# Optimization experiments

Measured on AMD Instinct MI355X. Metric: run time of the kernel, lower is better.

The kernel has to match this reference:

```python
import jax, jax.numpy as jnp
import numpy as np

EPS_BN = 1e-5

def conv1(W, x):
    # 1x1 conv1d, no bias: W (Cout,Cin), x (B,Cin,N)
    return jnp.einsum('oc,bcn->bon', W, x)

def bn(x, g, b):
    # training-mode BatchNorm1d over (batch, points) per channel
    m = jnp.mean(x, axis=(0, 2), keepdims=True)
    v = jnp.mean((x - m) ** 2, axis=(0, 2), keepdims=True)
    return g[None, :, None] * (x - m) / jnp.sqrt(v + EPS_BN) + b[None, :, None]

def three_interpolation(p_dense, p_sparse, f_sparse):
    # p_dense (B,N1,3), p_sparse (B,N2,3), f_sparse (B,C,N2) -> (B,C,N1)
    d2 = jnp.sum((p_dense[:, :, None, :] - p_sparse[:, None, :, :]) ** 2, axis=-1)  # (B,N1,N2)
    neg, idx = jax.lax.top_k(-d2, 3)  # 3 nearest neighbors, (B,N1,3)
    w = 1.0 / (jnp.maximum(-neg, 0.0) + 1e-8)  # inverse (squared) distance, as pointnet2 three_nn
    w = w / jnp.sum(w, axis=-1, keepdims=True)
    gathered = jax.vmap(lambda f, i: f[:, i])(f_sparse, idx)  # (B,C,N1,3)
    return jnp.einsum('bcnk,bnk->bcn', gathered, w)

def fp(p_dense, f_skip, p_sparse, f_sparse, W1, g1, b1, W2, g2, b2):
    # FeaturePropogation upsample branch: concat(skip, interp) -> [conv1d+BN] x decoder_layers (act_args=None)
    x = jnp.concatenate([f_skip, three_interpolation(p_dense, p_sparse, f_sparse)], axis=1)
    x = bn(conv1(W1, x), g1, b1)
    x = bn(conv1(W2, x), g2, b2)
    return x

def setup_inputs():
    key = jax.random.key(0)
    ks = iter(jax.random.split(key, 40))
    B, N = 4, 8192
    Ns = [N, N, 2048, 512, 128]      # point counts of p0..p4 (strides 4)
    Cs = [128, 256, 512, 1024]       # encoder_channel_list
    d = {}
    for i in range(5):
        d[f'p{i}'] = jax.random.normal(next(ks), (B, Ns[i], 3), jnp.float32)
    for i in range(4):
        d[f'f{i + 1}'] = jax.random.normal(next(ks), (B, Cs[i], Ns[i + 1]), jnp.float32)
    d['cls_label'] = jax.random.randint(next(ks), (B, 1), 0, 16)
    # class-label convs: 16 -> 64 (BN+GELU) -> C0
    d['Wc1'] = jax.random.normal(next(ks), (64, 16), jnp.float32) * 0.1
    d['gc'] = jax.random.uniform(next(ks), (64,), jnp.float32, 0.5, 1.5)
    d['bc'] = jax.random.normal(next(ks), (64,), jnp.float32) * 0.1
    d['Wc2'] = jax.random.normal(next(ks), (Cs[0], 64), jnp.float32) * 0.1
    # decoder stages, coarsest (s2) to finest (s0)
    ins = [Cs[2] + Cs[3], Cs[1] + Cs[2], Cs[0] + Cs[1]]
    outs = [Cs[2], Cs[1], Cs[0]]
    for tag, ci, co in zip(['s2', 's1', 's0'], ins, outs):
        d[f'W{tag}a'] = jax.random.normal(next(ks), (co, ci), jnp.float32) * 0.05
        d[f'g{tag}a'] = jax.random.uniform(next(ks), (co,), jnp.float32, 0.5, 1.5)
        d[f'b{tag}a'] = jax.random.normal(next(ks), (co,), jnp.float32) * 0.1
        d[f'W{tag}b'] = jax.random.normal(next(ks), (co, co), jnp.float32) * 0.05
        d[f'g{tag}b'] = jax.random.uniform(next(ks), (co,), jnp.float32, 0.5, 1.5)
        d[f'b{tag}b'] = jax.random.normal(next(ks), (co,), jnp.float32) * 0.1
    return d

def reference(p0, p1, p2, p3, p4, f1, f2, f3, f4, cls_label,
              Wc1, gc, bc, Wc2,
              Ws2a, gs2a, bs2a, Ws2b, gs2b, bs2b,
              Ws1a, gs1a, bs1a, Ws1b, gs1b, bs1b,
              Ws0a, gs0a, bs0a, Ws0b, gs0b, bs0b):
    B, N = p0.shape[0], p0.shape[1]
    # one-hot class embedding broadcast over points, mapped 16 -> 64 -> C0
    one_hot = jax.nn.one_hot(cls_label[:, 0], 16, dtype=f1.dtype)  # (B,16)
    cls_feat = jnp.broadcast_to(one_hot[:, :, None], (B, 16, N))
    cls_feat = conv1(Wc2, jax.nn.gelu(bn(conv1(Wc1, cls_feat), gc, bc), approximate=False))
    # decoder stages, coarse to fine
    f3n = fp(p3, f3, p4, f4, Ws2a, gs2a, bs2a, Ws2b, gs2b, bs2b)   # (B,512,512)
    f2n = fp(p2, f2, p3, f3n, Ws1a, gs1a, bs1a, Ws1b, gs1b, bs1b)  # (B,256,2048)
    f1n = fp(p1, f1 + cls_feat, p2, f2n, Ws0a, gs0a, bs0a, Ws0b, gs0b, bs0b)  # (B,128,8192)
    return f1n
```

## Files before the change

kernel.cpp:

```cpp
#include <hip/hip_runtime.h>
#include <math.h>

#define BN_EPS 1e-5f

typedef float f32x4 __attribute__((ext_vector_type(4)));
typedef short s16x8 __attribute__((ext_vector_type(8)));
typedef short s16x4 __attribute__((ext_vector_type(4)));

__device__ __forceinline__ unsigned short f2bf(float f) {
    unsigned u = __builtin_bit_cast(unsigned, f);
    u = u + 0x7FFFu + ((u >> 16) & 1u);
    return (unsigned short)(u >> 16);
}
__device__ __forceinline__ float bf2f(unsigned short s) {
    unsigned u = ((unsigned)s) << 16;
    return __builtin_bit_cast(float, u);
}

__device__ __forceinline__ void gload16(const void* g, void* l) {
    __builtin_amdgcn_global_load_lds((const __attribute__((address_space(1))) unsigned int*)g,
                                     (__attribute__((address_space(3))) unsigned int*)l,
                                     16, 0, 0);
}

__global__ __launch_bounds__(256) void tr_all(const float* __restrict__ f1,
                                              const float* __restrict__ f2,
                                              const float* __restrict__ f3,
                                              const float* __restrict__ f4,
                                              unsigned short* __restrict__ F1T,
                                              unsigned short* __restrict__ F2T,
                                              unsigned short* __restrict__ F3T,
                                              unsigned short* __restrict__ F4T,
                                              const int* __restrict__ lbl,
                                              const float* __restrict__ Wc1,
                                              const float* __restrict__ gc,
                                              const float* __restrict__ bc,
                                              const float* __restrict__ Wc2) {
    __shared__ float t[32][33];
    __shared__ float clsv[32];
    __shared__ float hsh[4][64];
    __shared__ float actsh[4][64];
    int bx = blockIdx.x, b = blockIdx.y;
    const float* in; unsigned short* out; int C, N, nx, seg; bool docls = false;
    if (bx < 128)      { in = f4; out = F4T; C = 1024; N = 128;  nx = 4;   seg = bx; }
    else if (bx < 384) { in = f3; out = F3T; C = 512;  N = 512;  nx = 16;  seg = bx - 128; }
    else if (bx < 896) { in = f2; out = F2T; C = 256;  N = 2048; nx = 64;  seg = bx - 384; }
    else               { in = f1; out = F1T; C = 128;  N = 8192; nx = 256; seg = bx - 896; docls = true; }
    int n0 = (seg % nx) * 32, c0 = (seg / nx) * 32;
    int tid = threadIdx.x;
    if (docls) {
        { int b2 = tid >> 6, c = tid & 63; hsh[b2][c] = Wc1[c * 16 + lbl[b2]]; }
        __syncthreads();
        if (tid < 64) {
            int c = tid;
            float m = 0.f;
            for (int b2 = 0; b2 < 4; b2++) m += hsh[b2][c];
            m *= 0.25f;
            float v = 0.f;
            for (int b2 = 0; b2 < 4; b2++) { float d = hsh[b2][c] - m; v += d * d; }
            v *= 0.25f;
            float sc = gc[c] * rsqrtf(v + BN_EPS);
            float sh = bc[c] - m * sc;
            for (int b2 = 0; b2 < 4; b2++) {
                float x = hsh[b2][c] * sc + sh;
                actsh[b2][c] = 0.5f * x * (1.f + erff(x * 0.70710678118654752f));
            }
        }
        __syncthreads();
        if (tid < 32) {
            float s = 0.f;
            for (int c = 0; c < 64; c++) s += Wc2[(size_t)(c0 + tid) * 64 + c] * actsh[b][c];
            clsv[tid] = s;
        }
        __syncthreads();
    }
    int i = tid & 31, jj = tid >> 5;
#pragma unroll
    for (int j = jj; j < 32; j += 8) {
        float v = in[((size_t)b * C + c0 + j) * N + n0 + i];
        if (docls) v += clsv[j];
        t[j][i] = v;
    }
    __syncthreads();
    int j2 = tid & 31, i2b = tid >> 5;
#pragma unroll
    for (int i2 = i2b; i2 < 32; i2 += 8)
        out[((size_t)b * N + n0 + i2) * C + c0 + j2] = f2bf(t[j2][i2]);
}

template<int CAND, int CHUNK, int STRIDE, bool PART>
__device__ __forceinline__ void knn_body(const float* __restrict__ pd,
                                         const float* __restrict__ ps,
                                         int N1, int N2total, int grp, int slice, int b,
                                         int* __restrict__ idx, float* __restrict__ w,
                                         unsigned long long* __restrict__ pk, int nslice,
                                         float* spx, float* spy, float* spz) {
    int tid = threadIdx.x;
    int cbase = slice * CAND;
    for (int g = tid; g < CAND; g += 256) {
        int s = g / CHUNK, off = g % CHUNK;
        size_t base = ((size_t)b * N2total + cbase + g) * 3;
        spx[s * STRIDE + off] = ps[base];
        spy[s * STRIDE + off] = ps[base + 1];
        spz[s * STRIDE + off] = ps[base + 2];
    }
    __syncthreads();
    int sub = tid & 7;
    int n = grp * 32 + (tid >> 3);
    size_t pb = ((size_t)b * N1 + n) * 3;
    float px = pd[pb], py = pd[pb + 1], pz = pd[pb + 2];
    float dd0 = 3.4e38f, dd1 = 3.4e38f, dd2 = 3.4e38f;
    int ii0 = 0, ii1 = 0, ii2 = 0;
    const float* rx = spx + sub * STRIDE;
    const float* ry = spy + sub * STRIDE;
    const float* rz = spz + sub * STRIDE;
    int jbase = cbase + sub * CHUNK;
    for (int t = 0; t < CHUNK; t += 4) {
        f32x4 x4 = *(const f32x4*)(rx + t);
        f32x4 y4 = *(const f32x4*)(ry + t);
        f32x4 z4 = *(const f32x4*)(rz + t);
#pragma unroll
        for (int e = 0; e < 4; e++) {
            float dx = px - x4[e], dy = py - y4[e], dz = pz - z4[e];
            float d = dx * dx + dy * dy + dz * dz;
            int j = jbase + t + e;
            bool C0 = d < dd0, C1 = d < dd1, C2 = d < dd2;
            int ni2 = C1 ? ii1 : (C2 ? j : ii2);
            int ni1 = C0 ? ii0 : (C1 ? j : ii1);
            int ni0 = C0 ? j : ii0;
            dd2 = __builtin_amdgcn_fmed3f(d, dd1, dd2);
            dd1 = __builtin_amdgcn_fmed3f(d, dd0, dd1);
            dd0 = fminf(d, dd0);
            ii0 = ni0; ii1 = ni1; ii2 = ni2;
        }
    }
    unsigned long long k0 = ((unsigned long long)__builtin_bit_cast(unsigned, dd0) << 32) | (unsigned)ii0;
    unsigned long long k1 = ((unsigned long long)__builtin_bit_cast(unsigned, dd1) << 32) | (unsigned)ii1;
    unsigned long long k2 = ((unsigned long long)__builtin_bit_cast(unsigned, dd2) << 32) | (unsigned)ii2;
#pragma unroll
    for (int m = 1; m < 8; m <<= 1) {
        unsigned long long e0, e1, e2;
        { int lo = __shfl_xor((int)(unsigned)(k0 & 0xFFFFFFFFull), m), hi = __shfl_xor((int)(unsigned)(k0 >> 32), m);
          e0 = ((unsigned long long)(unsigned)hi << 32) | (unsigned)lo; }
        { int lo = __shfl_xor((int)(unsigned)(k1 & 0xFFFFFFFFull), m), hi = __shfl_xor((int)(unsigned)(k1 >> 32), m);
          e1 = ((unsigned long long)(unsigned)hi << 32) | (unsigned)lo; }
        { int lo = __shfl_xor((int)(unsigned)(k2 & 0xFFFFFFFFull), m), hi = __shfl_xor((int)(unsigned)(k2 >> 32), m);
          e2 = ((unsigned long long)(unsigned)hi << 32) | (unsigned)lo; }
        unsigned long long t0, t1;
        t0 = k0 > e0 ? k0 : e0; k0 = k0 < e0 ? k0 : e0; t1 = k1 > t0 ? k1 : t0; k1 = k1 < t0 ? k1 : t0; k2 = k2 < t1 ? k2 : t1;
        t0 = k0 > e1 ? k0 : e1; k0 = k0 < e1 ? k0 : e1; t1 = k1 > t0 ? k1 : t0; k1 = k1 < t0 ? k1 : t0; k2 = k2 < t1 ? k2 : t1;
        t0 = k0 > e2 ? k0 : e2; k0 = k0 < e2 ? k0 : e2; t1 = k1 > t0 ? k1 : t0; k1 = k1 < t0 ? k1 : t0; k2 = k2 < t1 ? k2 : t1;
    }
    if (sub == 0) {
        if (PART) {
            size_t o = ((size_t)(b * N1 + n) * nslice + slice) * 3;
            pk[o] = k0; pk[o + 1] = k1; pk[o + 2] = k2;
        } else {
            float f0 = __builtin_bit_cast(float, (unsigned)(k0 >> 32));
            float f1 = __builtin_bit_cast(float, (unsigned)(k1 >> 32));
            float f2 = __builtin_bit_cast(float, (unsigned)(k2 >> 32));
            float w0 = 1.f / (f0 + 1e-8f), w1 = 1.f / (f1 + 1e-8f), w2 = 1.f / (f2 + 1e-8f);
            float s = 1.f / (w0 + w1 + w2);
            size_t o = ((size_t)b * N1 + n) * 3;
            idx[o] = (int)(unsigned)(k0 & 0xFFFFFFFFull);
            idx[o + 1] = (int)(unsigned)(k1 & 0xFFFFFFFFull);
            idx[o + 2] = (int)(unsigned)(k2 & 0xFFFFFFFFull);
            w[o] = w0 * s; w[o + 1] = w1 * s; w[o + 2] = w2 * s;
        }
    }
}

__global__ __launch_bounds__(256) void knn_part(const float* __restrict__ p1,
                                                const float* __restrict__ p2,
                                                const float* __restrict__ p3,
                                                const float* __restrict__ p4,
                                                int* __restrict__ idx1, float* __restrict__ w1,
                                                int* __restrict__ idx2, float* __restrict__ w2,
                                                unsigned long long* __restrict__ pk0) {
    __shared__ float spx[8 * 72], spy[8 * 72], spz[8 * 72];
    int bx = blockIdx.x, b = blockIdx.y;
    if (bx < 16)      knn_body<128, 16, 24, false>(p3, p4, 512, 128, bx, 0, b, idx2, w2, nullptr, 1, spx, spy, spz);
    else if (bx < 80) knn_body<512, 64, 72, false>(p2, p3, 2048, 512, bx - 16, 0, b, idx1, w1, nullptr, 1, spx, spy, spz);
    else {
        int u = bx - 80;
        knn_body<512, 64, 72, true>(p1, p2, 8192, 2048, u >> 2, u & 3, b, nullptr, nullptr, pk0, 4, spx, spy, spz);
    }
}

__global__ __launch_bounds__(256) void knn_merge(const unsigned long long* __restrict__ pk,
                                                 int* __restrict__ idx, float* __restrict__ w,
                                                 int NQ) {
    int q = blockIdx.x * 256 + threadIdx.x;
    if (q >= NQ) return;
    const unsigned long long* p = pk + (size_t)q * 12;
    unsigned long long k0 = ~0ull, k1 = ~0ull, k2 = ~0ull;
#pragma unroll
    for (int i = 0; i < 12; i++) {
        unsigned long long c = p[i];
        unsigned long long t0 = k0 > c ? k0 : c; k0 = k0 < c ? k0 : c;
        unsigned long long t1 = k1 > t0 ? k1 : t0; k1 = k1 < t0 ? k1 : t0;
        k2 = k2 < t1 ? k2 : t1;
    }
    float f0 = __builtin_bit_cast(float, (unsigned)(k0 >> 32));
    float f1 = __builtin_bit_cast(float, (unsigned)(k1 >> 32));
    float f2 = __builtin_bit_cast(float, (unsigned)(k2 >> 32));
    float w0 = 1.f / (f0 + 1e-8f), w1 = 1.f / (f1 + 1e-8f), w2 = 1.f / (f2 + 1e-8f);
    float s = 1.f / (w0 + w1 + w2);
    size_t o = (size_t)q * 3;
    idx[o] = (int)(unsigned)(k0 & 0xFFFFFFFFull);
    idx[o + 1] = (int)(unsigned)(k1 & 0xFFFFFFFFull);
    idx[o + 2] = (int)(unsigned)(k2 & 0xFFFFFFFFull);
    w[o] = w0 * s; w[o + 1] = w1 * s; w[o + 2] = w2 * s;
}

__global__ __launch_bounds__(256) void interp_y(const unsigned short* __restrict__ GT,
                                                const int* __restrict__ idx,
                                                const float* __restrict__ w,
                                                unsigned short* __restrict__ out,
                                                int M, int N1, int N2) {
    int mq = M >> 3;
    size_t gid = (size_t)blockIdx.x * 256 + threadIdx.x;
    if (gid >= (size_t)4 * N1 * mq) return;
    int c = (int)(gid % mq) * 8;
    int n = (int)((gid / mq) % N1);
    int b = (int)(gid / ((size_t)mq * N1));
    size_t ob = ((size_t)b * N1 + n) * 3;
    int i0 = idx[ob], i1 = idx[ob + 1], i2 = idx[ob + 2];
    float w0 = w[ob], w1 = w[ob + 1], w2 = w[ob + 2];
    s16x8 v0 = *(const s16x8*)(GT + ((size_t)b * N2 + i0) * M + c);
    s16x8 v1 = *(const s16x8*)(GT + ((size_t)b * N2 + i1) * M + c);
    s16x8 v2 = *(const s16x8*)(GT + ((size_t)b * N2 + i2) * M + c);
    s16x8 o;
#pragma unroll
    for (int j = 0; j < 8; j++) {
        float v = w0 * bf2f((unsigned short)v0[j]) + w1 * bf2f((unsigned short)v1[j]) + w2 * bf2f((unsigned short)v2[j]);
        o[j] = (short)f2bf(v);
    }
    *(s16x8*)(out + ((size_t)b * N1 + n) * M + c) = o;
}

__global__ __launch_bounds__(256) void wprep(const float* __restrict__ W,
                                             const float* __restrict__ sc,
                                             const float* __restrict__ sh,
                                             unsigned short* __restrict__ Wb,
                                             float* __restrict__ bias,
                                             int Ktot, int kOff, int Ks) {
    int m = blockIdx.x;
    int tid = threadIdx.x;
    float bsum = 0.f;
    for (int k = tid; k < Ks; k += 256) {
        float wv = W[(size_t)m * Ktot + kOff + k];
        float o = wv;
        if (sc) {
            o = wv * sc[k];
            bsum += wv * sh[k];
        }
        Wb[(size_t)m * Ks + k] = f2bf(o);
    }
    __shared__ float ls[256];
    ls[tid] = bsum;
    __syncthreads();
    for (int o = 128; o > 0; o >>= 1) {
        if (tid < o) ls[tid] += ls[tid + o];
        __syncthreads();
    }
    if (tid == 0) bias[m] = ls[0];
}

template<bool PRE>
__global__ __launch_bounds__(256) void gemm64(const unsigned short* __restrict__ XT,
                                              const unsigned short* __restrict__ Wb,
                                              const float* __restrict__ bias,
                                              const unsigned short* __restrict__ pre,
                                              unsigned short* __restrict__ OutT,
                                              float* __restrict__ ps,
                                              int BN, int K, int M) {
    __shared__ unsigned short As[2][64 * 32];
    __shared__ unsigned short Bs[2][64 * 32];
    __shared__ float sred[2][2][32][2];
    int tid = threadIdx.x;
    int lane = tid & 63, wid = tid >> 6;
    int wn = wid & 1, wm = wid >> 1;
    int bx = blockIdx.x, by = blockIdx.y;

    int srow = (wid << 4) + (lane >> 2);
    int skcol = (lane & 3) << 3;
    const unsigned short* gA = XT + (size_t)(bx * 64 + srow) * K + skcol;
    const unsigned short* gB = Wb + (size_t)(by * 64 + srow) * K + skcol;

    int r16 = lane & 15, q = lane >> 4;
    f32x4 acc[2][2];
    if (PRE) {
        const unsigned short* Pb = pre + (size_t)(bx * 64) * M + by * 64;
#pragma unroll
        for (int i = 0; i < 2; i++)
#pragma unroll
            for (int j = 0; j < 2; j++) {
                int mcol = wm * 32 + j * 16 + r16;
#pragma unroll
                for (int r = 0; r < 4; r++) {
                    int n = wn * 32 + i * 16 + q * 4 + r;
                    acc[i][j][r] = bf2f(Pb[(size_t)n * M + mcol]);
                }
            }
    } else {
#pragma unroll
        for (int i = 0; i < 2; i++)
#pragma unroll
            for (int j = 0; j < 2; j++) acc[i][j] = (f32x4)0.f;
    }

    int nt = K >> 5;
    gload16(gA, &As[0][wid * 512]);
    gload16(gB, &Bs[0][wid * 512]);

    for (int t = 0; t < nt; t++) {
        int cur = t & 1;
        if (t + 1 < nt) {
            int k0 = (t + 1) << 5;
            gload16(gA + k0, &As[cur ^ 1][wid * 512]);
            gload16(gB + k0, &Bs[cur ^ 1][wid * 512]);
            asm volatile("s_waitcnt vmcnt(2)" ::: "memory");
        } else {
            asm volatile("s_waitcnt vmcnt(0)" ::: "memory");
        }
        __syncthreads();
        s16x8 afr[2], bfr[2];
        afr[0] = *(const s16x8*)&As[cur][(wn * 32 + r16) * 32 + q * 8];
        afr[1] = *(const s16x8*)&As[cur][(wn * 32 + 16 + r16) * 32 + q * 8];
        bfr[0] = *(const s16x8*)&Bs[cur][(wm * 32 + r16) * 32 + q * 8];
        bfr[1] = *(const s16x8*)&Bs[cur][(wm * 32 + 16 + r16) * 32 + q * 8];
        asm volatile("s_waitcnt lgkmcnt(0)" ::: "memory");
        __builtin_amdgcn_sched_barrier(0);
        __syncthreads();
#pragma unroll
        for (int i = 0; i < 2; i++)
#pragma unroll
            for (int j = 0; j < 2; j++)
                acc[i][j] = __builtin_amdgcn_mfma_f32_16x16x32_bf16(afr[i], bfr[j], acc[i][j], 0, 0, 0);
    }

    int mc0 = by * 64 + wm * 32 + r16;
    float bv[2] = { bias[mc0], bias[mc0 + 16] };
    unsigned short* Ob = OutT + (size_t)(bx * 64) * M + by * 64;
    float s[2] = {0.f, 0.f}, qq[2] = {0.f, 0.f};
#pragma unroll
    for (int i = 0; i < 2; i++) {
#pragma unroll
        for (int j = 0; j < 2; j++) {
            int mcol = wm * 32 + j * 16 + r16;
#pragma unroll
            for (int r = 0; r < 4; r++) {
                float v = acc[i][j][r] + bv[j];
                s[j] += v; qq[j] += v * v;
                int n = wn * 32 + i * 16 + q * 4 + r;
                Ob[(size_t)n * M + mcol] = f2bf(v);
            }
        }
    }
#pragma unroll
    for (int j = 0; j < 2; j++) {
        s[j] += __shfl_xor(s[j], 16); s[j] += __shfl_xor(s[j], 32);
        qq[j] += __shfl_xor(qq[j], 16); qq[j] += __shfl_xor(qq[j], 32);
    }
    if (lane < 16) {
#pragma unroll
        for (int j = 0; j < 2; j++) {
            sred[wn][wm][j * 16 + lane][0] = s[j];
            sred[wn][wm][j * 16 + lane][1] = qq[j];
        }
    }
    __syncthreads();
    if (tid < 64) {
        int wmm = tid >> 5, c = tid & 31;
        float ssum = sred[0][wmm][c][0] + sred[1][wmm][c][0];
        float qsum = sred[0][wmm][c][1] + sred[1][wmm][c][1];
        size_t blin = (size_t)by * gridDim.x + bx;
        ps[blin * 128 + tid * 2] = ssum;
        ps[blin * 128 + tid * 2 + 1] = qsum;
    }
}

__global__ __launch_bounds__(256) void bn_finalize(const float* __restrict__ ps,
                                                   const float* __restrict__ g,
                                                   const float* __restrict__ bb,
                                                   float* __restrict__ sc,
                                                   float* __restrict__ sh,
                                                   int gx, int Npts) {
    int m = blockIdx.x;
    int by = m >> 6, ch = m & 63;
    float s = 0.f, q = 0.f;
    for (int bxi = threadIdx.x; bxi < gx; bxi += 256) {
        size_t blin = (size_t)by * gx + bxi;
        s += ps[blin * 128 + ch * 2];
        q += ps[blin * 128 + ch * 2 + 1];
    }
    __shared__ float ls[256], lq[256];
    ls[threadIdx.x] = s; lq[threadIdx.x] = q;
    __syncthreads();
    for (int o = 128; o > 0; o >>= 1) {
        if (threadIdx.x < o) { ls[threadIdx.x] += ls[threadIdx.x + o]; lq[threadIdx.x] += lq[threadIdx.x + o]; }
        __syncthreads();
    }
    if (threadIdx.x == 0) {
        float inv = 1.f / (float)Npts;
        float mean = ls[0] * inv;
        float var = fmaxf(lq[0] * inv - mean * mean, 0.f);
        float scale = g[m] * rsqrtf(var + BN_EPS);
        sc[m] = scale;
        sh[m] = bb[m] - mean * scale;
    }
}

__global__ __launch_bounds__(256) void out_bn_tr(const unsigned short* __restrict__ in,
                                                 float* __restrict__ out,
                                                 const float* __restrict__ sc,
                                                 const float* __restrict__ sh,
                                                 int M, int N) {
    __shared__ float t[32][33];
    int b = blockIdx.z;
    int n0 = blockIdx.x * 32, m0 = blockIdx.y * 32;
    int j = threadIdx.x & 31, ii = threadIdx.x >> 5;
#pragma unroll
    for (int i = ii; i < 32; i += 8)
        t[i][j] = bf2f(in[((size_t)b * N + n0 + i) * M + m0 + j]);
    __syncthreads();
    int i2 = threadIdx.x & 31, j2b = threadIdx.x >> 5;
#pragma unroll
    for (int j2 = j2b; j2 < 32; j2 += 8)
        out[((size_t)b * M + m0 + j2) * N + n0 + i2] = t[i2][j2] * sc[m0 + j2] + sh[m0 + j2];
}

extern "C" void kernel_launch(void* const* d_in, const int* in_sizes, int n_in,
                              void* d_out, int out_size, void* d_ws, size_t ws_size,
                              hipStream_t stream) {
    const float* p1 = (const float*)d_in[1];
    const float* p2 = (const float*)d_in[2];
    const float* p3 = (const float*)d_in[3];
    const float* p4 = (const float*)d_in[4];
    const float* f1 = (const float*)d_in[5];
    const float* f2 = (const float*)d_in[6];
    const float* f3 = (const float*)d_in[7];
    const float* f4 = (const float*)d_in[8];
    const int* cls = (const int*)d_in[9];
    const float* Wc1 = (const float*)d_in[10];
    const float* gc  = (const float*)d_in[11];
    const float* bc  = (const float*)d_in[12];
    const float* Wc2 = (const float*)d_in[13];
    const float* Ws2a = (const float*)d_in[14];
    const float* gs2a = (const float*)d_in[15];
    const float* bs2a = (const float*)d_in[16];
    const float* Ws2b = (const float*)d_in[17];
    const float* gs2b = (const float*)d_in[18];
    const float* bs2b = (const float*)d_in[19];
    const float* Ws1a = (const float*)d_in[20];
    const float* gs1a = (const float*)d_in[21];
    const float* bs1a = (const float*)d_in[22];
    const float* Ws1b = (const float*)d_in[23];
    const float* gs1b = (const float*)d_in[24];
    const float* bs1b = (const float*)d_in[25];
    const float* Ws0a = (const float*)d_in[26];
    const float* gs0a = (const float*)d_in[27];
    const float* bs0a = (const float*)d_in[28];
    const float* Ws0b = (const float*)d_in[29];
    const float* gs0b = (const float*)d_in[30];
    const float* bs0b = (const float*)d_in[31];

    char* ws = (char*)d_ws;
    size_t off = 0;
    auto alloc = [&](size_t bytes) { char* p = ws + off; off += (bytes + 255) & ~(size_t)255; return p; };
    unsigned short* F4T = (unsigned short*)alloc((size_t)4 * 128 * 1024 * 2);
    unsigned short* F3T = (unsigned short*)alloc((size_t)4 * 512 * 512 * 2);
    unsigned short* F2T = (unsigned short*)alloc((size_t)4 * 2048 * 256 * 2);
    unsigned short* F1T = (unsigned short*)alloc((size_t)4 * 8192 * 128 * 2);
    unsigned short* G2T = (unsigned short*)alloc((size_t)4 * 128 * 512 * 2);
    unsigned short* G1T = (unsigned short*)alloc((size_t)4 * 512 * 256 * 2);
    unsigned short* G0T = (unsigned short*)alloc((size_t)4 * 2048 * 128 * 2);
    unsigned short* YI2 = (unsigned short*)alloc((size_t)4 * 512 * 512 * 2);
    unsigned short* YI1 = (unsigned short*)alloc((size_t)4 * 2048 * 256 * 2);
    unsigned short* YI0 = (unsigned short*)alloc((size_t)4 * 8192 * 128 * 2);
    unsigned short* YA  = (unsigned short*)alloc((size_t)4 * 8192 * 128 * 2);
    unsigned short* FN2 = (unsigned short*)alloc((size_t)4 * 512 * 512 * 2);
    unsigned short* FN1 = (unsigned short*)alloc((size_t)4 * 2048 * 256 * 2);
    unsigned short* XO  = (unsigned short*)alloc((size_t)4 * 8192 * 128 * 2);
    unsigned short* WI2 = (unsigned short*)alloc((size_t)512 * 1024 * 2);
    unsigned short* WS2 = (unsigned short*)alloc((size_t)512 * 512 * 2);
    unsigned short* WB2b = (unsigned short*)alloc((size_t)512 * 512 * 2);
    unsigned short* WI1 = (unsigned short*)alloc((size_t)256 * 512 * 2);
    unsigned short* WS1 = (unsigned short*)alloc((size_t)256 * 256 * 2);
    unsigned short* WB1b = (unsigned short*)alloc((size_t)256 * 256 * 2);
    unsigned short* WI0 = (unsigned short*)alloc((size_t)128 * 256 * 2);
    unsigned short* WS0 = (unsigned short*)alloc((size_t)128 * 128 * 2);
    unsigned short* WB0b = (unsigned short*)alloc((size_t)128 * 128 * 2);
    float* BIA2 = (float*)alloc(512 * 4); float* BIS2 = (float*)alloc(512 * 4);
    float* BI2b = (float*)alloc(512 * 4);
    float* BIA1 = (float*)alloc(256 * 4); float* BIS1 = (float*)alloc(256 * 4);
    float* BI1b = (float*)alloc(256 * 4);
    float* BIA0 = (float*)alloc(128 * 4); float* BIS0 = (float*)alloc(128 * 4);
    float* BI0b = (float*)alloc(128 * 4);
    int*   IDX0 = (int*)alloc((size_t)4 * 8192 * 3 * 4);
    float* WGT0 = (float*)alloc((size_t)4 * 8192 * 3 * 4);
    int*   IDX1 = (int*)alloc((size_t)4 * 2048 * 3 * 4);
    float* WGT1 = (float*)alloc((size_t)4 * 2048 * 3 * 4);
    int*   IDX2 = (int*)alloc((size_t)4 * 512 * 3 * 4);
    float* WGT2 = (float*)alloc((size_t)4 * 512 * 3 * 4);
    unsigned long long* PK0 = (unsigned long long*)alloc((size_t)4 * 8192 * 4 * 3 * 8);
    float* PS = (float*)alloc((size_t)1024 * 128 * 4);
    float* SC2a = (float*)alloc(512 * 4); float* SH2a = (float*)alloc(512 * 4);
    float* SC2b = (float*)alloc(512 * 4); float* SH2b = (float*)alloc(512 * 4);
    float* SC1a = (float*)alloc(512 * 4); float* SH1a = (float*)alloc(512 * 4);
    float* SC1b = (float*)alloc(512 * 4); float* SH1b = (float*)alloc(512 * 4);
    float* SC0a = (float*)alloc(512 * 4); float* SH0a = (float*)alloc(512 * 4);
    float* SC0b = (float*)alloc(512 * 4); float* SH0b = (float*)alloc(512 * 4);
    float* OUT = (float*)d_out;

    tr_all<<<dim3(1920, 4), 256, 0, stream>>>(f1, f2, f3, f4, F1T, F2T, F3T, F4T, cls, Wc1, gc, bc, Wc2);
    knn_part<<<dim3(1104, 4), 256, 0, stream>>>(p1, p2, p3, p4, IDX1, WGT1, IDX2, WGT2, PK0);
    knn_merge<<<(4 * 8192) / 256, 256, 0, stream>>>(PK0, IDX0, WGT0, 4 * 8192);
    wprep<<<512, 256, 0, stream>>>(Ws2a, nullptr, nullptr, WI2, BIA2, 1536, 512, 1024);
    wprep<<<512, 256, 0, stream>>>(Ws2a, nullptr, nullptr, WS2, BIS2, 1536, 0, 512);
    wprep<<<256, 256, 0, stream>>>(Ws1a, nullptr, nullptr, WS1, BIS1, 768, 0, 256);
    wprep<<<128, 256, 0, stream>>>(Ws0a, nullptr, nullptr, WS0, BIS0, 384, 0, 128);

    gemm64<false><<<dim3(8, 8), 256, 0, stream>>>(F4T, WI2, BIA2, nullptr, G2T, PS, 512, 1024, 512);
    interp_y<<<(4 * 512 * (512 / 8) + 255) / 256, 256, 0, stream>>>(G2T, IDX2, WGT2, YI2, 512, 512, 128);
    gemm64<true><<<dim3(32, 8), 256, 0, stream>>>(F3T, WS2, BIS2, YI2, YA, PS, 2048, 512, 512);
    bn_finalize<<<512, 256, 0, stream>>>(PS, gs2a, bs2a, SC2a, SH2a, 32, 2048);
    wprep<<<512, 256, 0, stream>>>(Ws2b, SC2a, SH2a, WB2b, BI2b, 512, 0, 512);
    gemm64<false><<<dim3(32, 8), 256, 0, stream>>>(YA, WB2b, BI2b, nullptr, FN2, PS, 2048, 512, 512);
    bn_finalize<<<512, 256, 0, stream>>>(PS, gs2b, bs2b, SC2b, SH2b, 32, 2048);

    wprep<<<256, 256, 0, stream>>>(Ws1a, SC2b, SH2b, WI1, BIA1, 768, 256, 512);
    gemm64<false><<<dim3(32, 4), 256, 0, stream>>>(FN2, WI1, BIA1, nullptr, G1T, PS, 2048, 512, 256);
    interp_y<<<(4 * 2048 * (256 / 8) + 255) / 256, 256, 0, stream>>>(G1T, IDX1, WGT1, YI1, 256, 2048, 512);
    gemm64<true><<<dim3(128, 4), 256, 0, stream>>>(F2T, WS1, BIS1, YI1, YA, PS, 8192, 256, 256);
    bn_finalize<<<256, 256, 0, stream>>>(PS, gs1a, bs1a, SC1a, SH1a, 128, 8192);
    wprep<<<256, 256, 0, stream>>>(Ws1b, SC1a, SH1a, WB1b, BI1b, 256, 0, 256);
    gemm64<false><<<dim3(128, 4), 256, 0, stream>>>(YA, WB1b, BI1b, nullptr, FN1, PS, 8192, 256, 256);
    bn_finalize<<<256, 256, 0, stream>>>(PS, gs1b, bs1b, SC1b, SH1b, 128, 8192);

    wprep<<<128, 256, 0, stream>>>(Ws0a, SC1b, SH1b, WI0, BIA0, 384, 128, 256);
    gemm64<false><<<dim3(128, 2), 256, 0, stream>>>(FN1, WI0, BIA0, nullptr, G0T, PS, 8192, 256, 128);
    interp_y<<<(4 * 8192 * (128 / 8) + 255) / 256, 256, 0, stream>>>(G0T, IDX0, WGT0, YI0, 128, 8192, 2048);
    gemm64<true><<<dim3(512, 2), 256, 0, stream>>>(F1T, WS0, BIS0, YI0, YA, PS, 32768, 128, 128);
    bn_finalize<<<128, 256, 0, stream>>>(PS, gs0a, bs0a, SC0a, SH0a, 512, 32768);
    wprep<<<128, 256, 0, stream>>>(Ws0b, SC0a, SH0a, WB0b, BI0b, 128, 0, 128);
    gemm64<false><<<dim3(512, 2), 256, 0, stream>>>(YA, WB0b, BI0b, nullptr, XO, PS, 32768, 128, 128);
    bn_finalize<<<128, 256, 0, stream>>>(PS, gs0b, bs0b, SC0b, SH0b, 512, 32768);

    out_bn_tr<<<dim3(8192 / 32, 128 / 32, 4), 256, 0, stream>>>(XO, OUT, SC0b, SH0b, 128, 8192);
}
```

Measured before the change: 205.6 us.

## Fuse prep kernels, gather interpolation into GEMM epilogue, last-block BN finalize

Transpose, kNN and the first-layer weight conversion now run in one prep launch. The three-NN interpolation gather moves into the GEMM epilogue, so the separate interp_y kernel and its intermediate buffers are gone. BN statistics are finalized by the last block of each GEMM, found with an atomic counter, which replaces the bn_finalize launches. This removes many kernel launches and an intermediate round trip through memory. The cost is scattered per-element gather loads inside the GEMM and a serial reduction in a single block.

```diff
diff --git a/kernel.cpp b/kernel.cpp
--- a/kernel.cpp
+++ b/kernel.cpp
@@ -5,7 +5,6 @@
 
 typedef float f32x4 __attribute__((ext_vector_type(4)));
 typedef short s16x8 __attribute__((ext_vector_type(8)));
-typedef short s16x4 __attribute__((ext_vector_type(4)));
 
 __device__ __forceinline__ unsigned short f2bf(float f) {
     unsigned u = __builtin_bit_cast(unsigned, f);
@@ -21,71 +20,6 @@
     __builtin_amdgcn_global_load_lds((const __attribute__((address_space(1))) unsigned int*)g,
                                      (__attribute__((address_space(3))) unsigned int*)l,
                                      16, 0, 0);
-}
-
-__global__ __launch_bounds__(256) void tr_all(const float* __restrict__ f1,
-                                              const float* __restrict__ f2,
-                                              const float* __restrict__ f3,
-                                              const float* __restrict__ f4,
-                                              unsigned short* __restrict__ F1T,
-                                              unsigned short* __restrict__ F2T,
-                                              unsigned short* __restrict__ F3T,
-                                              unsigned short* __restrict__ F4T,
-                                              const int* __restrict__ lbl,
-                                              const float* __restrict__ Wc1,
-                                              const float* __restrict__ gc,
-                                              const float* __restrict__ bc,
-                                              const float* __restrict__ Wc2) {
-    __shared__ float t[32][33];
-    __shared__ float clsv[32];
-    __shared__ float hsh[4][64];
-    __shared__ float actsh[4][64];
-    int bx = blockIdx.x, b = blockIdx.y;
-    const float* in; unsigned short* out; int C, N, nx, seg; bool docls = false;
-    if (bx < 128)      { in = f4; out = F4T; C = 1024; N = 128;  nx = 4;   seg = bx; }
-    else if (bx < 384) { in = f3; out = F3T; C = 512;  N = 512;  nx = 16;  seg = bx - 128; }
-    else if (bx < 896) { in = f2; out = F2T; C = 256;  N = 2048; nx = 64;  seg = bx - 384; }
-    else               { in = f1; out = F1T; C = 128;  N = 8192; nx = 256; seg = bx - 896; docls = true; }
-    int n0 = (seg % nx) * 32, c0 = (seg / nx) * 32;
-    int tid = threadIdx.x;
-    if (docls) {
-        { int b2 = tid >> 6, c = tid & 63; hsh[b2][c] = Wc1[c * 16 + lbl[b2]]; }
-        __syncthreads();
-        if (tid < 64) {
-            int c = tid;
-            float m = 0.f;
-            for (int b2 = 0; b2 < 4; b2++) m += hsh[b2][c];
-            m *= 0.25f;
-            float v = 0.f;
-            for (int b2 = 0; b2 < 4; b2++) { float d = hsh[b2][c] - m; v += d * d; }
-            v *= 0.25f;
-            float sc = gc[c] * rsqrtf(v + BN_EPS);
-            float sh = bc[c] - m * sc;
-            for (int b2 = 0; b2 < 4; b2++) {
-                float x = hsh[b2][c] * sc + sh;
-                actsh[b2][c] = 0.5f * x * (1.f + erff(x * 0.70710678118654752f));
-            }
-        }
-        __syncthreads();
-        if (tid < 32) {
-            float s = 0.f;
-            for (int c = 0; c < 64; c++) s += Wc2[(size_t)(c0 + tid) * 64 + c] * actsh[b][c];
-            clsv[tid] = s;
-        }
-        __syncthreads();
-    }
-    int i = tid & 31, jj = tid >> 5;
-#pragma unroll
-    for (int j = jj; j < 32; j += 8) {
-        float v = in[((size_t)b * C + c0 + j) * N + n0 + i];
-        if (docls) v += clsv[j];
-        t[j][i] = v;
-    }
-    __syncthreads();
-    int j2 = tid & 31, i2b = tid >> 5;
-#pragma unroll
-    for (int i2 = i2b; i2 < 32; i2 += 8)
-        out[((size_t)b * N + n0 + i2) * C + c0 + j2] = f2bf(t[j2][i2]);
 }
 
 template<int CAND, int CHUNK, int STRIDE, bool PART>
@@ -170,21 +104,108 @@
     }
 }
 
-__global__ __launch_bounds__(256) void knn_part(const float* __restrict__ p1,
-                                                const float* __restrict__ p2,
-                                                const float* __restrict__ p3,
-                                                const float* __restrict__ p4,
-                                                int* __restrict__ idx1, float* __restrict__ w1,
-                                                int* __restrict__ idx2, float* __restrict__ w2,
-                                                unsigned long long* __restrict__ pk0) {
+__global__ __launch_bounds__(256) void prep(const float* __restrict__ f1,
+                                            const float* __restrict__ f2,
+                                            const float* __restrict__ f3,
+                                            const float* __restrict__ f4,
+                                            unsigned short* __restrict__ F1T,
+                                            unsigned short* __restrict__ F2T,
+                                            unsigned short* __restrict__ F3T,
+                                            unsigned short* __restrict__ F4T,
+                                            const int* __restrict__ lbl,
+                                            const float* __restrict__ Wc1,
+                                            const float* __restrict__ gc,
+                                            const float* __restrict__ bc,
+                                            const float* __restrict__ Wc2,
+                                            const float* __restrict__ p1,
+                                            const float* __restrict__ p2,
+                                            const float* __restrict__ p3,
+                                            const float* __restrict__ p4,
+                                            int* __restrict__ idx1, float* __restrict__ w1,
+                                            int* __restrict__ idx2, float* __restrict__ w2,
+                                            unsigned long long* __restrict__ pk0,
+                                            const float* __restrict__ Ws2a,
+                                            unsigned short* __restrict__ WI2, float* __restrict__ BIA2,
+                                            unsigned short* __restrict__ WS2, float* __restrict__ BIS2,
+                                            const float* __restrict__ Ws1a,
+                                            unsigned short* __restrict__ WS1, float* __restrict__ BIS1,
+                                            const float* __restrict__ Ws0a,
+                                            unsigned short* __restrict__ WS0, float* __restrict__ BIS0) {
+    __shared__ float t[32][33];
+    __shared__ float clsv[32];
+    __shared__ float hsh[4][64];
+    __shared__ float actsh[4][64];
     __shared__ float spx[8 * 72], spy[8 * 72], spz[8 * 72];
     int bx = blockIdx.x, b = blockIdx.y;
-    if (bx < 16)      knn_body<128, 16, 24, false>(p3, p4, 512, 128, bx, 0, b, idx2, w2, nullptr, 1, spx, spy, spz);
-    else if (bx < 80) knn_body<512, 64, 72, false>(p2, p3, 2048, 512, bx - 16, 0, b, idx1, w1, nullptr, 1, spx, spy, spz);
-    else {
-        int u = bx - 80;
-        knn_body<512, 64, 72, true>(p1, p2, 8192, 2048, u >> 2, u & 3, b, nullptr, nullptr, pk0, 4, spx, spy, spz);
-    }
+    int tid = threadIdx.x;
+
+    if (bx >= 3024) {
+        if (b != 0) return;
+        int wx = bx - 3024;
+        const float* W; unsigned short* Wb; float* bias; int Ktot, kOff, Ks, m;
+        if (wx < 512)       { W = Ws2a; Wb = WI2; bias = BIA2; Ktot = 1536; kOff = 512; Ks = 1024; m = wx; }
+        else if (wx < 1024) { W = Ws2a; Wb = WS2; bias = BIS2; Ktot = 1536; kOff = 0;   Ks = 512;  m = wx - 512; }
+        else if (wx < 1280) { W = Ws1a; Wb = WS1; bias = BIS1; Ktot = 768;  kOff = 0;   Ks = 256;  m = wx - 1024; }
+        else                { W = Ws0a; Wb = WS0; bias = BIS0; Ktot = 384;  kOff = 0;   Ks = 128;  m = wx - 1280; }
+        for (int k = tid; k < Ks; k += 256)
+            Wb[(size_t)m * Ks + k] = f2bf(W[(size_t)m * Ktot + kOff + k]);
+        if (tid == 0) bias[m] = 0.f;
+        return;
+    }
+    if (bx >= 1920) {
+        int kx = bx - 1920;
+        if (kx < 16)      knn_body<128, 16, 24, false>(p3, p4, 512, 128, kx, 0, b, idx2, w2, nullptr, 1, spx, spy, spz);
+        else if (kx < 80) knn_body<512, 64, 72, false>(p2, p3, 2048, 512, kx - 16, 0, b, idx1, w1, nullptr, 1, spx, spy, spz);
+        else {
+            int u = kx - 80;
+            knn_body<512, 64, 72, true>(p1, p2, 8192, 2048, u >> 2, u & 3, b, nullptr, nullptr, pk0, 4, spx, spy, spz);
+        }
+        return;
+    }
+    const float* in; unsigned short* out; int C, N, nx, seg; bool docls = false;
+    if (bx < 128)      { in = f4; out = F4T; C = 1024; N = 128;  nx = 4;   seg = bx; }
+    else if (bx < 384) { in = f3; out = F3T; C = 512;  N = 512;  nx = 16;  seg = bx - 128; }
+    else if (bx < 896) { in = f2; out = F2T; C = 256;  N = 2048; nx = 64;  seg = bx - 384; }
+    else               { in = f1; out = F1T; C = 128;  N = 8192; nx = 256; seg = bx - 896; docls = true; }
+    int n0 = (seg % nx) * 32, c0 = (seg / nx) * 32;
+    if (docls) {
+        { int b2 = tid >> 6, c = tid & 63; hsh[b2][c] = Wc1[c * 16 + lbl[b2]]; }
+        __syncthreads();
+        if (tid < 64) {
+            int c = tid;
+            float m = 0.f;
+            for (int b2 = 0; b2 < 4; b2++) m += hsh[b2][c];
+            m *= 0.25f;
+            float v = 0.f;
+            for (int b2 = 0; b2 < 4; b2++) { float d = hsh[b2][c] - m; v += d * d; }
+            v *= 0.25f;
+            float sc = gc[c] * rsqrtf(v + BN_EPS);
+            float sh = bc[c] - m * sc;
+            for (int b2 = 0; b2 < 4; b2++) {
+                float x = hsh[b2][c] * sc + sh;
+                actsh[b2][c] = 0.5f * x * (1.f + erff(x * 0.70710678118654752f));
+            }
+        }
+        __syncthreads();
+        if (tid < 32) {
+            float s = 0.f;
+            for (int c = 0; c < 64; c++) s += Wc2[(size_t)(c0 + tid) * 64 + c] * actsh[b][c];
+            clsv[tid] = s;
+        }
+        __syncthreads();
+    }
+    int i = tid & 31, jj = tid >> 5;
+#pragma unroll
+    for (int j = jj; j < 32; j += 8) {
+        float v = in[((size_t)b * C + c0 + j) * N + n0 + i];
+        if (docls) v += clsv[j];
+        t[j][i] = v;
+    }
+    __syncthreads();
+    int j2 = tid & 31, i2b = tid >> 5;
+#pragma unroll
+    for (int i2 = i2b; i2 < 32; i2 += 8)
+        out[((size_t)b * N + n0 + i2) * C + c0 + j2] = f2bf(t[j2][i2]);
 }
 
 __global__ __launch_bounds__(256) void knn_merge(const unsigned long long* __restrict__ pk,
@@ -211,32 +232,6 @@
     idx[o + 1] = (int)(unsigned)(k1 & 0xFFFFFFFFull);
     idx[o + 2] = (int)(unsigned)(k2 & 0xFFFFFFFFull);
     w[o] = w0 * s; w[o + 1] = w1 * s; w[o + 2] = w2 * s;
-}
-
-__global__ __launch_bounds__(256) void interp_y(const unsigned short* __restrict__ GT,
-                                                const int* __restrict__ idx,
-                                                const float* __restrict__ w,
-                                                unsigned short* __restrict__ out,
-                                                int M, int N1, int N2) {
-    int mq = M >> 3;
-    size_t gid = (size_t)blockIdx.x * 256 + threadIdx.x;
-    if (gid >= (size_t)4 * N1 * mq) return;
-    int c = (int)(gid % mq) * 8;
-    int n = (int)((gid / mq) % N1);
-    int b = (int)(gid / ((size_t)mq * N1));
-    size_t ob = ((size_t)b * N1 + n) * 3;
-    int i0 = idx[ob], i1 = idx[ob + 1], i2 = idx[ob + 2];
-    float w0 = w[ob], w1 = w[ob + 1], w2 = w[ob + 2];
-    s16x8 v0 = *(const s16x8*)(GT + ((size_t)b * N2 + i0) * M + c);
-    s16x8 v1 = *(const s16x8*)(GT + ((size_t)b * N2 + i1) * M + c);
-    s16x8 v2 = *(const s16x8*)(GT + ((size_t)b * N2 + i2) * M + c);
-    s16x8 o;
-#pragma unroll
-    for (int j = 0; j < 8; j++) {
-        float v = w0 * bf2f((unsigned short)v0[j]) + w1 * bf2f((unsigned short)v1[j]) + w2 * bf2f((unsigned short)v2[j]);
-        o[j] = (short)f2bf(v);
-    }
-    *(s16x8*)(out + ((size_t)b * N1 + n) * M + c) = o;
 }
 
 __global__ __launch_bounds__(256) void wprep(const float* __restrict__ W,
@@ -250,12 +245,8 @@
     float bsum = 0.f;
     for (int k = tid; k < Ks; k += 256) {
         float wv = W[(size_t)m * Ktot + kOff + k];
-        float o = wv;
-        if (sc) {
-            o = wv * sc[k];
-            bsum += wv * sh[k];
-        }
-        Wb[(size_t)m * Ks + k] = f2bf(o);
+        Wb[(size_t)m * Ks + k] = f2bf(wv * sc[k]);
+        bsum += wv * sh[k];
     }
     __shared__ float ls[256];
     ls[tid] = bsum;
@@ -267,17 +258,26 @@
     if (tid == 0) bias[m] = ls[0];
 }
 
-template<bool PRE>
+template<bool GATHER, bool STATS>
 __global__ __launch_bounds__(256) void gemm64(const unsigned short* __restrict__ XT,
                                               const unsigned short* __restrict__ Wb,
                                               const float* __restrict__ bias,
-                                              const unsigned short* __restrict__ pre,
+                                              const unsigned short* __restrict__ G,
+                                              const int* __restrict__ gidx,
+                                              const float* __restrict__ gw,
+                                              int n1shift, int N2loc,
                                               unsigned short* __restrict__ OutT,
                                               float* __restrict__ ps,
+                                              const float* __restrict__ bng,
+                                              const float* __restrict__ bnb,
+                                              float* __restrict__ scOut,
+                                              float* __restrict__ shOut,
+                                              unsigned* __restrict__ cnt, int Npts,
                                               int BN, int K, int M) {
     __shared__ unsigned short As[2][64 * 32];
     __shared__ unsigned short Bs[2][64 * 32];
     __shared__ float sred[2][2][32][2];
+    __shared__ int lastFlag;
     int tid = threadIdx.x;
     int lane = tid & 63, wid = tid >> 6;
     int wn = wid & 1, wm = wid >> 1;
@@ -290,25 +290,10 @@
 
     int r16 = lane & 15, q = lane >> 4;
     f32x4 acc[2][2];
-    if (PRE) {
-        const unsigned short* Pb = pre + (size_t)(bx * 64) * M + by * 64;
-#pragma unroll
-        for (int i = 0; i < 2; i++)
-#pragma unroll
-            for (int j = 0; j < 2; j++) {
-                int mcol = wm * 32 + j * 16 + r16;
-#pragma unroll
-                for (int r = 0; r < 4; r++) {
-                    int n = wn * 32 + i * 16 + q * 4 + r;
-                    acc[i][j][r] = bf2f(Pb[(size_t)n * M + mcol]);
-                }
-            }
-    } else {
-#pragma unroll
-        for (int i = 0; i < 2; i++)
-#pragma unroll
-            for (int j = 0; j < 2; j++) acc[i][j] = (f32x4)0.f;
-    }
+#pragma unroll
+    for (int i = 0; i < 2; i++)
+#pragma unroll
+        for (int j = 0; j < 2; j++) acc[i][j] = (f32x4)0.f;
 
     int nt = K >> 5;
     gload16(gA, &As[0][wid * 512]);
@@ -340,6 +325,27 @@
                 acc[i][j] = __builtin_amdgcn_mfma_f32_16x16x32_bf16(afr[i], bfr[j], acc[i][j], 0, 0, 0);
     }
 
+    if (GATHER) {
+#pragma unroll
+        for (int i = 0; i < 2; i++)
+#pragma unroll
+            for (int rr = 0; rr < 4; rr++) {
+                int R = bx * 64 + wn * 32 + i * 16 + q * 4 + rr;
+                size_t ob = (size_t)R * 3;
+                int i0 = gidx[ob], i1 = gidx[ob + 1], i2 = gidx[ob + 2];
+                float w0 = gw[ob], w1 = gw[ob + 1], w2 = gw[ob + 2];
+                size_t gbase = (size_t)(R >> n1shift) * N2loc;
+                const unsigned short* g0 = G + (gbase + i0) * M + by * 64;
+                const unsigned short* g1 = G + (gbase + i1) * M + by * 64;
+                const unsigned short* g2 = G + (gbase + i2) * M + by * 64;
+#pragma unroll
+                for (int j = 0; j < 2; j++) {
+                    int mcol = wm * 32 + j * 16 + r16;
+                    acc[i][j][rr] += w0 * bf2f(g0[mcol]) + w1 * bf2f(g1[mcol]) + w2 * bf2f(g2[mcol]);
+                }
+            }
+    }
+
     int mc0 = by * 64 + wm * 32 + r16;
     float bv[2] = { bias[mc0], bias[mc0 + 16] };
     unsigned short* Ob = OutT + (size_t)(bx * 64) * M + by * 64;
@@ -358,57 +364,56 @@
             }
         }
     }
-#pragma unroll
-    for (int j = 0; j < 2; j++) {
-        s[j] += __shfl_xor(s[j], 16); s[j] += __shfl_xor(s[j], 32);
-        qq[j] += __shfl_xor(qq[j], 16); qq[j] += __shfl_xor(qq[j], 32);
-    }
-    if (lane < 16) {
+    if (STATS) {
 #pragma unroll
         for (int j = 0; j < 2; j++) {
-            sred[wn][wm][j * 16 + lane][0] = s[j];
-            sred[wn][wm][j * 16 + lane][1] = qq[j];
-        }
-    }
-    __syncthreads();
-    if (tid < 64) {
-        int wmm = tid >> 5, c = tid & 31;
-        float ssum = sred[0][wmm][c][0] + sred[1][wmm][c][0];
-        float qsum = sred[0][wmm][c][1] + sred[1][wmm][c][1];
-        size_t blin = (size_t)by * gridDim.x + bx;
-        ps[blin * 128 + tid * 2] = ssum;
-        ps[blin * 128 + tid * 2 + 1] = qsum;
-    }
-}
-
-__global__ __launch_bounds__(256) void bn_finalize(const float* __restrict__ ps,
-                                                   const float* __restrict__ g,
-                                                   const float* __restrict__ bb,
-                                                   float* __restrict__ sc,
-                                                   float* __restrict__ sh,
-                                                   int gx, int Npts) {
-    int m = blockIdx.x;
-    int by = m >> 6, ch = m & 63;
-    float s = 0.f, q = 0.f;
-    for (int bxi = threadIdx.x; bxi < gx; bxi += 256) {
-        size_t blin = (size_t)by * gx + bxi;
-        s += ps[blin * 128 + ch * 2];
-        q += ps[blin * 128 + ch * 2 + 1];
-    }
-    __shared__ float ls[256], lq[256];
-    ls[threadIdx.x] = s; lq[threadIdx.x] = q;
-    __syncthreads();
-    for (int o = 128; o > 0; o >>= 1) {
-        if (threadIdx.x < o) { ls[threadIdx.x] += ls[threadIdx.x + o]; lq[threadIdx.x] += lq[threadIdx.x + o]; }
-        __syncthreads();
-    }
-    if (threadIdx.x == 0) {
-        float inv = 1.f / (float)Npts;
-        float mean = ls[0] * inv;
-        float var = fmaxf(lq[0] * inv - mean * mean, 0.f);
-        float scale = g[m] * rsqrtf(var + BN_EPS);
-        sc[m] = scale;
-        sh[m] = bb[m] - mean * scale;
+            s[j] += __shfl_xor(s[j], 16); s[j] += __shfl_xor(s[j], 32);
+            qq[j] += __shfl_xor(qq[j], 16); qq[j] += __shfl_xor(qq[j], 32);
+        }
+        if (lane < 16) {
+#pragma unroll
+            for (int j = 0; j < 2; j++) {
+                sred[wn][wm][j * 16 + lane][0] = s[j];
+                sred[wn][wm][j * 16 + lane][1] = qq[j];
+            }
+        }
+        __syncthreads();
+        if (tid < 64) {
+            int wmm = tid >> 5, c = tid & 31;
+            float ssum = sred[0][wmm][c][0] + sred[1][wmm][c][0];
+            float qsum = sred[0][wmm][c][1] + sred[1][wmm][c][1];
+            size_t blin = (size_t)by * gridDim.x + bx;
+            ps[blin * 128 + tid * 2] = ssum;
+            ps[blin * 128 + tid * 2 + 1] = qsum;
+        }
+        __syncthreads();
+        if (tid == 0) {
+            __threadfence();
+            unsigned total = gridDim.x * gridDim.y;
+            unsigned old = atomicAdd(cnt, 1u);
+            lastFlag = (old == total - 1) ? 1 : 0;
+        }
+        __syncthreads();
+        if (lastFlag) {
+            __threadfence();
+            int gx = gridDim.x;
+            for (int m = tid; m < M; m += 256) {
+                int byy = m >> 6, ch = m & 63;
+                float ssum = 0.f, qsum = 0.f;
+                for (int bxi = 0; bxi < gx; bxi++) {
+                    size_t blin = (size_t)byy * gx + bxi;
+                    ssum += ps[blin * 128 + ch * 2];
+                    qsum += ps[blin * 128 + ch * 2 + 1];
+                }
+                float inv = 1.f / (float)Npts;
+                float mean = ssum * inv;
+                float var = fmaxf(qsum * inv - mean * mean, 0.f);
+                float scale = bng[m] * rsqrtf(var + BN_EPS);
+                scOut[m] = scale;
+                shOut[m] = bnb[m] - mean * scale;
+            }
+            if (tid == 0) *cnt = 0u;
+        }
     }
 }
 
@@ -476,9 +481,6 @@
     unsigned short* G2T = (unsigned short*)alloc((size_t)4 * 128 * 512 * 2);
     unsigned short* G1T = (unsigned short*)alloc((size_t)4 * 512 * 256 * 2);
     unsigned short* G0T = (unsigned short*)alloc((size_t)4 * 2048 * 128 * 2);
-    unsigned short* YI2 = (unsigned short*)alloc((size_t)4 * 512 * 512 * 2);
-    unsigned short* YI1 = (unsigned short*)alloc((size_t)4 * 2048 * 256 * 2);
-    unsigned short* YI0 = (unsigned short*)alloc((size_t)4 * 8192 * 128 * 2);
     unsigned short* YA  = (unsigned short*)alloc((size_t)4 * 8192 * 128 * 2);
     unsigned short* FN2 = (unsigned short*)alloc((size_t)4 * 512 * 512 * 2);
     unsigned short* FN1 = (unsigned short*)alloc((size_t)4 * 2048 * 256 * 2);
@@ -506,6 +508,7 @@
     float* WGT2 = (float*)alloc((size_t)4 * 512 * 3 * 4);
     unsigned long long* PK0 = (unsigned long long*)alloc((size_t)4 * 8192 * 4 * 3 * 8);
     float* PS = (float*)alloc((size_t)1024 * 128 * 4);
+    unsigned* CNT = (unsigned*)alloc(8 * 4);
     float* SC2a = (float*)alloc(512 * 4); float* SH2a = (float*)alloc(512 * 4);
     float* SC2b = (float*)alloc(512 * 4); float* SH2b = (float*)alloc(512 * 4);
     float* SC1a = (float*)alloc(512 * 4); float* SH1a = (float*)alloc(512 * 4);
@@ -514,39 +517,50 @@
     float* SC0b = (float*)alloc(512 * 4); float* SH0b = (float*)alloc(512 * 4);
     float* OUT = (float*)d_out;
 
-    tr_all<<<dim3(1920, 4), 256, 0, stream>>>(f1, f2, f3, f4, F1T, F2T, F3T, F4T, cls, Wc1, gc, bc, Wc2);
-    knn_part<<<dim3(1104, 4), 256, 0, stream>>>(p1, p2, p3, p4, IDX1, WGT1, IDX2, WGT2, PK0);
+    hipMemsetAsync(CNT, 0, 8 * 4, stream);
+
+    prep<<<dim3(4432, 4), 256, 0, stream>>>(f1, f2, f3, f4, F1T, F2T, F3T, F4T,
+                                            cls, Wc1, gc, bc, Wc2,
+                                            p1, p2, p3, p4,
+                                            IDX1, WGT1, IDX2, WGT2, PK0,
+                                            Ws2a, WI2, BIA2, WS2, BIS2,
+                                            Ws1a, WS1, BIS1, Ws0a, WS0, BIS0);
     knn_merge<<<(4 * 8192) / 256, 256, 0, stream>>>(PK0, IDX0, WGT0, 4 * 8192);
-    wprep<<<512, 256, 0, stream>>>(Ws2a, nullptr, nullptr, WI2, BIA2, 1536, 512, 1024);
-    wprep<<<512, 256, 0, stream>>>(Ws2a, nullptr, nullptr, WS2, BIS2, 1536, 0, 512);
-    wprep<<<256, 256, 0, stream>>>(Ws1a, nullptr, nullptr, WS1, BIS1, 768, 0, 256);
-    wprep<<<128, 256, 0, stream>>>(Ws0a, nullptr, nullptr, WS0, BIS0, 384, 0, 128);
-
-    gemm64<false><<<dim3(8, 8), 256, 0, stream>>>(F4T, WI2, BIA2, nullptr, G2T, PS, 512, 1024, 512);
-    interp_y<<<(4 * 512 * (512 / 8) + 255) / 256, 256, 0, stream>>>(G2T, IDX2, WGT2, YI2, 512, 512, 128);
-    gemm64<true><<<dim3(32, 8), 256, 0, stream>>>(F3T, WS2, BIS2, YI2, YA, PS, 2048, 512, 512);
-    bn_finalize<<<512, 256, 0, stream>>>(PS, gs2a, bs2a, SC2a, SH2a, 32, 2048);
+
+    gemm64<false, false><<<dim3(8, 8), 256, 0, stream>>>(F4T, WI2, BIA2, nullptr, nullptr, nullptr, 0, 0,
+                                                         G2T, nullptr, nullptr, nullptr, nullptr, nullptr, nullptr, 0,
+                                                         512, 1024, 512);
+    gemm64<true, true><<<dim3(32, 8), 256, 0, stream>>>(F3T, WS2, BIS2, G2T, IDX2, WGT2, 9, 128,
+                                                        YA, PS, gs2a, bs2a, SC2a, SH2a, CNT + 0, 2048,
+                                                        2048, 512, 512);
     wprep<<<512, 256, 0, stream>>>(Ws2b, SC2a, SH2a, WB2b, BI2b, 512, 0, 512);
-    gemm64<false><<<dim3(32, 8), 256, 0, stream>>>(YA, WB2b, BI2b, nullptr, FN2, PS, 2048, 512, 512);
-    bn_finalize<<<512, 256, 0, stream>>>(PS, gs2b, bs2b, SC2b, SH2b, 32, 2048);
+    gemm64<false, true><<<dim3(32, 8), 256, 0, stream>>>(YA, WB2b, BI2b, nullptr, nullptr, nullptr, 0, 0,
+                                                         FN2, PS, gs2b, bs2b, SC2b, SH2b, CNT + 1, 2048,
+                                                         2048, 512, 512);
 
     wprep<<<256, 256, 0, stream>>>(Ws1a, SC2b, SH2b, WI1, BIA1, 768, 256, 512);
-    gemm64<false><<<dim3(32, 4), 256, 0, stream>>>(FN2, WI1, BIA1, nullptr, G1T, PS, 2048, 512, 256);
-    interp_y<<<(4 * 2048 * (256 / 8) + 255) / 256, 256, 0, stream>>>(G1T, IDX1, WGT1, YI1, 256, 2048, 512);
-    gemm64<true><<<dim3(128, 4), 256, 0, stream>>>(F2T, WS1, BIS1, YI1, YA, PS, 8192, 256, 256);
-    bn_finalize<<<256, 256, 0, stream>>>(PS, gs1a, bs1a, SC1a, SH1a, 128, 8192);
+    gemm64<false, false><<<dim3(32, 4), 256, 0, stream>>>(FN2, WI1, BIA1, nullptr, nullptr, nullptr, 0, 0,
+                                                          G1T, nullptr, nullptr, nullptr, nullptr, nullptr, nullptr, 0,
+                                                          2048, 512, 256);
+    gemm64<true, true><<<dim3(128, 4), 256, 0, stream>>>(F2T, WS1, BIS1, G1T, IDX1, WGT1, 11, 512,
+                                                         YA, PS, gs1a, bs1a, SC1a, SH1a, CNT + 2, 8192,
+                                                         8192, 256, 256);
     wprep<<<256, 256, 0, stream>>>(Ws1b, SC1a, SH1a, WB1b, BI1b, 256, 0, 256);
-    gemm64<false><<<dim3(128, 4), 256, 0, stream>>>(YA, WB1b, BI1b, nullptr, FN1, PS, 8192, 256, 256);
-    bn_finalize<<<256, 256, 0, stream>>>(PS, gs1b, bs1b, SC1b, SH1b, 128, 8192);
+    gemm64<false, true><<<dim3(128, 4), 256, 0, stream>>>(YA, WB1b, BI1b, nullptr, nullptr, nullptr, 0, 0,
+                                                          FN1, PS, gs1b, bs1b, SC1b, SH1b, CNT + 3, 8192,
+                                                          8192, 256, 256);
 
     wprep<<<128, 256, 0, stream>>>(Ws0a, SC1b, SH1b, WI0, BIA0, 384, 128, 256);
-    gemm64<false><<<dim3(128, 2), 256, 0, stream>>>(FN1, WI0, BIA0, nullptr, G0T, PS, 8192, 256, 128);
-    interp_y<<<(4 * 8192 * (128 / 8) + 255) / 256, 256, 0, stream>>>(G0T, IDX0, WGT0, YI0, 128, 8192, 2048);
-    gemm64<true><<<dim3(512, 2), 256, 0, stream>>>(F1T, WS0, BIS0, YI0, YA, PS, 32768, 128, 128);
-    bn_finalize<<<128, 256, 0, stream>>>(PS, gs0a, bs0a, SC0a, SH0a, 512, 32768);
+    gemm64<false, false><<<dim3(128, 2), 256, 0, stream>>>(FN1, WI0, BIA0, nullptr, nullptr, nullptr, 0, 0,
+                                                           G0T, nullptr, nullptr, nullptr, nullptr, nullptr, nullptr, 0,
+                                                           8192, 256, 128);
+    gemm64<true, true><<<dim3(512, 2), 256, 0, stream>>>(F1T, WS0, BIS0, G0T, IDX0, WGT0, 13, 2048,
+                                                         YA, PS, gs0a, bs0a, SC0a, SH0a, CNT + 4, 32768,
+                                                         32768, 128, 128);
     wprep<<<128, 256, 0, stream>>>(Ws0b, SC0a, SH0a, WB0b, BI0b, 128, 0, 128);
-    gemm64<false><<<dim3(512, 2), 256, 0, stream>>>(YA, WB0b, BI0b, nullptr, XO, PS, 32768, 128, 128);
-    bn_finalize<<<128, 256, 0, stream>>>(PS, gs0b, bs0b, SC0b, SH0b, 512, 32768);
+    gemm64<false, true><<<dim3(512, 2), 256, 0, stream>>>(YA, WB0b, BI0b, nullptr, nullptr, nullptr, 0, 0,
+                                                          XO, PS, gs0b, bs0b, SC0b, SH0b, CNT + 5, 32768,
+                                                          32768, 128, 128);
 
     out_bn_tr<<<dim3(8192 / 32, 128 / 32, 4), 256, 0, stream>>>(XO, OUT, SC0b, SH0b, 128, 8192);
 }
```

After: 641.5 us. 212% more time.
